# Kernel optimization log

Measured on AMD Instinct MI355X. Metric: run time of the kernel, lower is better.

## Reference

```python
import jax, jax.numpy as jnp
import numpy as np

H = 1024  # hidden_size == embedding_size


def setup_inputs() -> dict:
    key = jax.random.key(0)
    ks = jax.random.split(key, 14)
    B, T, L, V = 2, 1, 8192, 50000
    emb_table = jax.random.normal(ks[0], (V, H), jnp.float32)
    emb_table = emb_table.at[0].set(0.0)  # row 0 zeroed as in the torch module
    return {
        "input_ids": jax.random.randint(ks[1], (B, T), 0, V),
        "last_context": jax.random.normal(ks[2], (B, T, H), jnp.float32),
        "last_hidden": jax.random.normal(ks[3], (1, B, H), jnp.float32),
        "encoder_outputs": jax.random.normal(ks[4], (B, L, H), jnp.float32),
        "emb_table": emb_table,
        "w_ih": jax.random.normal(ks[5], (3 * H, 2 * H), jnp.float32) * 0.02,
        "w_hh": jax.random.normal(ks[6], (3 * H, H), jnp.float32) * 0.02,
        "b_ih": jax.random.normal(ks[7], (3 * H,), jnp.float32) * 0.02,
        "b_hh": jax.random.normal(ks[8], (3 * H,), jnp.float32) * 0.02,
        "attn_w": jax.random.normal(ks[9], (H, 2 * H), jnp.float32) * 0.02,
        "attn_b": jax.random.normal(ks[10], (H,), jnp.float32) * 0.02,
        "v": jax.random.normal(ks[11], (H,), jnp.float32),
        "out_w": jax.random.normal(ks[12], (50000, 2 * H), jnp.float32) * 0.02,
        "out_b": jax.random.normal(ks[13], (50000,), jnp.float32) * 0.02,
    }


def _forward(input_ids, last_context, last_hidden, encoder_outputs, emb_table,
             w_ih, w_hh, b_ih, b_hh, attn_w, attn_b, v, out_w, out_b):
    # Embedding lookup (dropout p=0 -> identity)
    embedded = emb_table[input_ids]                      # [B,1,H]
    rnn_in = jnp.concatenate([embedded, last_context], -1)  # [B,1,2H]

    # Single-step, single-layer GRU (torch gate order: r, z, n)
    x = rnn_in[:, 0]                                     # [B,2H]
    h = last_hidden[0]                                   # [B,H]
    gx = x @ w_ih.T + b_ih                               # [B,3H]
    gh = h @ w_hh.T + b_hh                               # [B,3H]
    r = jax.nn.sigmoid(gx[:, :H] + gh[:, :H])
    z = jax.nn.sigmoid(gx[:, H:2 * H] + gh[:, H:2 * H])
    n = jnp.tanh(gx[:, 2 * H:] + r * gh[:, 2 * H:])
    h_new = (1.0 - z) * n + z * h                        # [B,H]
    rnn_output = h_new[:, None, :]                       # [B,1,H]
    hidden = h_new[None]                                 # [1,B,H]

    # Bahdanau 'concat' attention, vectorized over the seq_len loop:
    # energy[b,i] = v . (attn_w @ concat(h_new[b], enc[b,i]) + attn_b)
    w_h, w_e = attn_w[:, :H], attn_w[:, H:]
    e_h = h_new @ w_h.T + attn_b                         # [B,H]
    e_e = jnp.einsum('blh,kh->blk', encoder_outputs, w_e)  # [B,L,H]
    energies = jnp.einsum('blk,k->bl', e_e + e_h[:, None, :], v)  # [B,L]
    attn_weights = jax.nn.softmax(energies, axis=1)      # [B,L]
    context = jnp.einsum('bl,blh->bh', attn_weights, encoder_outputs)[:, None, :]  # [B,1,H]

    # Output projection over concat(rnn_output, context)
    cat = jnp.concatenate([rnn_output, context], -1)     # [B,1,2H]
    output = cat @ out_w.T + out_b                       # [B,1,V]
    return output, context, hidden, embedded, rnn_output


def reference(input_ids, last_context, last_hidden, encoder_outputs, emb_table,
              w_ih, w_hh, b_ih, b_hh, attn_w, attn_b, v, out_w, out_b):
    return _forward(input_ids, last_context, last_hidden, encoder_outputs, emb_table,
                    w_ih, w_hh, b_ih, b_hh, attn_w, attn_b, v, out_w, out_b)
```

## Files before the change

kernel.cpp:

```cpp
#include <hip/hip_runtime.h>

#define H 1024
#define B2 2
#define LEN 8192
#define V 50000

__device__ __forceinline__ float dot4(float4 a, float4 b) {
    return a.x * b.x + a.y * b.y + a.z * b.z + a.w * b.w;
}

__global__ void k_upart_emb(const float* __restrict__ attn_w,
                            const float* __restrict__ v,
                            float* __restrict__ upart,
                            const int* __restrict__ ids,
                            const float* __restrict__ emb,
                            float* __restrict__ out_emb) {
    int bid = blockIdx.x;
    int t   = threadIdx.x;
    if (bid < 64) {
        int h  = (bid & 3) * 256 + t;
        int kc = bid >> 2;
        float acc = 0.f;
#pragma unroll 8
        for (int i = 0; i < 64; ++i) {
            int k = kc * 64 + i;
            acc += v[k] * attn_w[(long)k * (2 * H) + H + h];
        }
        upart[kc * H + h] = acc;
    } else {
        int idx = (bid - 64) * 256 + t;
        int b = idx >> 10, h = idx & 1023;
        out_emb[idx] = emb[(long)ids[b] * H + h];
    }
}

__global__ void k_ured(const float* __restrict__ upart,
                       float* __restrict__ u) {
    int h = blockIdx.x * 256 + threadIdx.x;
    float acc = 0.f;
#pragma unroll
    for (int kc = 0; kc < 16; ++kc) acc += upart[kc * H + h];
    u[h] = acc;
}

__global__ void k_gru_energy(const int* __restrict__ ids,
                             const float* __restrict__ emb,
                             const float* __restrict__ lctx,
                             const float* __restrict__ lhid,
                             const float* __restrict__ w_ih,
                             const float* __restrict__ w_hh,
                             const float* __restrict__ b_ih,
                             const float* __restrict__ b_hh,
                             const float* __restrict__ enc,
                             const float* __restrict__ u,
                             float* __restrict__ o_hidden,
                             float* __restrict__ o_rnn,
                             float* __restrict__ en) {
    __shared__ float lds[3][4][4];
    int t = threadIdx.x;

    if (blockIdx.x >= 1024) {
        int row  = ((blockIdx.x - 1024) << 2) + (t >> 6);
        int lane = t & 63;
        const float* e = enc + (long)row * H;
        float acc = 0.f;
#pragma unroll
        for (int c = 0; c < 4; ++c) {
            int k = c * 256 + lane * 4;
            float4 ev = *(const float4*)(e + k);
            float4 uv = *(const float4*)(u + k);
            acc += dot4(ev, uv);
        }
        for (int off = 32; off; off >>= 1) acc += __shfl_down(acc, off, 64);
        if (lane == 0) en[row] = acc;
        return;
    }

    int hh = blockIdx.x;
    int kb = t * 8;

    float4 x0a, x0b, x1a, x1b;
    if (kb < H) {
        const float* p0 = emb + (long)ids[0] * H + kb;
        const float* p1 = emb + (long)ids[1] * H + kb;
        x0a = *(const float4*)p0;       x0b = *(const float4*)(p0 + 4);
        x1a = *(const float4*)p1;       x1b = *(const float4*)(p1 + 4);
    } else {
        const float* p0 = lctx + (kb - H);
        const float* p1 = lctx + H + (kb - H);
        x0a = *(const float4*)p0;       x0b = *(const float4*)(p0 + 4);
        x1a = *(const float4*)p1;       x1b = *(const float4*)(p1 + 4);
    }
    int kb2 = t * 4;
    float4 h0 = *(const float4*)(lhid + kb2);
    float4 h1 = *(const float4*)(lhid + H + kb2);

    for (int g = 0; g < 3; ++g) {
        const float* wi = w_ih + ((long)g * H + hh) * (2 * H) + kb;
        const float* wh = w_hh + ((long)g * H + hh) * H + kb2;
        float4 wa = *(const float4*)wi;
        float4 wb = *(const float4*)(wi + 4);
        float4 wc = *(const float4*)wh;
        float a0 = dot4(wa, x0a) + dot4(wb, x0b);
        float a1 = dot4(wa, x1a) + dot4(wb, x1b);
        float c0 = dot4(wc, h0);
        float c1 = dot4(wc, h1);
        for (int off = 32; off; off >>= 1) {
            a0 += __shfl_down(a0, off, 64);
            a1 += __shfl_down(a1, off, 64);
            c0 += __shfl_down(c0, off, 64);
            c1 += __shfl_down(c1, off, 64);
        }
        if ((t & 63) == 0) {
            int w = t >> 6;
            lds[g][w][0] = a0; lds[g][w][1] = a1;
            lds[g][w][2] = c0; lds[g][w][3] = c1;
        }
    }
    __syncthreads();
    if (t == 0) {
        float gx[3][2], gh[3][2];
        for (int g = 0; g < 3; ++g) {
            float s0 = 0, s1 = 0, s2 = 0, s3 = 0;
            for (int w = 0; w < 4; ++w) {
                s0 += lds[g][w][0]; s1 += lds[g][w][1];
                s2 += lds[g][w][2]; s3 += lds[g][w][3];
            }
            float bi = b_ih[g * H + hh], bh = b_hh[g * H + hh];
            gx[g][0] = s0 + bi; gx[g][1] = s1 + bi;
            gh[g][0] = s2 + bh; gh[g][1] = s3 + bh;
        }
        for (int b = 0; b < B2; ++b) {
            float r  = 1.f / (1.f + expf(-(gx[0][b] + gh[0][b])));
            float z  = 1.f / (1.f + expf(-(gx[1][b] + gh[1][b])));
            float n  = tanhf(gx[2][b] + r * gh[2][b]);
            float hp = lhid[b * H + hh];
            float hn = (1.f - z) * n + z * hp;
            o_hidden[b * H + hh] = hn;
            o_rnn[b * H + hh]    = hn;
        }
    }
}

__global__ void k_ctx(const float* __restrict__ enc,
                      const float* __restrict__ en,
                      float* __restrict__ part) {
    int b  = blockIdx.x >> 7;
    int lc = blockIdx.x & 127;
    int t  = threadIdx.x;
    const float* e_row = en + b * LEN;

    __shared__ float red[4];
    __shared__ float wlds[64];

    float m = -3.4e38f;
    for (int i = t; i < LEN; i += 256) m = fmaxf(m, e_row[i]);
    for (int off = 32; off; off >>= 1) m = fmaxf(m, __shfl_xor(m, off, 64));
    if ((t & 63) == 0) red[t >> 6] = m;
    __syncthreads();
    m = fmaxf(fmaxf(red[0], red[1]), fmaxf(red[2], red[3]));

    float s = 0.f;
    for (int i = t; i < LEN; i += 256) s += expf(e_row[i] - m);
    for (int off = 32; off; off >>= 1) s += __shfl_xor(s, off, 64);
    __syncthreads();
    if ((t & 63) == 0) red[t >> 6] = s;
    __syncthreads();
    float inv = 1.f / (red[0] + red[1] + red[2] + red[3]);

    if (t < 64) wlds[t] = expf(e_row[lc * 64 + t] - m) * inv;
    __syncthreads();

    const float* e = enc + ((long)b * LEN + lc * 64) * H + t * 4;
    float4 acc = {0.f, 0.f, 0.f, 0.f};
#pragma unroll 4
    for (int i = 0; i < 64; ++i) {
        float w = wlds[i];
        float4 ev = *(const float4*)(e + (long)i * H);
        acc.x += w * ev.x; acc.y += w * ev.y; acc.z += w * ev.z; acc.w += w * ev.w;
    }
    *(float4*)(part + (long)blockIdx.x * H + t * 4) = acc;
}

__global__ void k_ctx_red(const float* __restrict__ part,
                          float* __restrict__ out_ctx) {
    int idx = blockIdx.x * 256 + threadIdx.x;
    int b = idx >> 10, h = idx & 1023;
    float acc = 0.f;
#pragma unroll 8
    for (int lc = 0; lc < 128; ++lc) acc += part[((b << 7) + lc) * H + h];
    out_ctx[idx] = acc;
}

__global__ void k_out(const float* __restrict__ ow,
                      const float* __restrict__ ob,
                      const float* __restrict__ hnew,
                      const float* __restrict__ ctx,
                      float* __restrict__ out) {
    int t    = threadIdx.x;
    int lane = t & 63;
    int wv   = t >> 6;
    long row = (long)blockIdx.x * 4 + wv;

    float4 c0[8], c1[8];
#pragma unroll
    for (int j = 0; j < 4; ++j) {
        int k = (lane + 64 * j) * 4;
        c0[j] = *(const float4*)(hnew + k);
        c1[j] = *(const float4*)(hnew + H + k);
    }
#pragma unroll
    for (int j = 4; j < 8; ++j) {
        int k = (lane + 64 * j) * 4 - H;
        c0[j] = *(const float4*)(ctx + k);
        c1[j] = *(const float4*)(ctx + H + k);
    }

    const float4* w4 = (const float4*)(ow + row * (2 * H));
    float a0 = 0.f, a1 = 0.f;
#pragma unroll
    for (int j = 0; j < 8; ++j) {
        float4 w = w4[lane + 64 * j];
        a0 += dot4(w, c0[j]);
        a1 += dot4(w, c1[j]);
    }
    for (int off = 32; off; off >>= 1) {
        a0 += __shfl_down(a0, off, 64);
        a1 += __shfl_down(a1, off, 64);
    }
    if (lane == 0) {
        float bb = ob[row];
        out[row]     = a0 + bb;
        out[V + row] = a1 + bb;
    }
}

extern "C" void kernel_launch(void* const* d_in, const int* in_sizes, int n_in,
                              void* d_out, int out_size, void* d_ws, size_t ws_size,
                              hipStream_t stream) {
    const int*   ids    = (const int*)  d_in[0];
    const float* lctx   = (const float*)d_in[1];
    const float* lhid   = (const float*)d_in[2];
    const float* enc    = (const float*)d_in[3];
    const float* emb    = (const float*)d_in[4];
    const float* w_ih   = (const float*)d_in[5];
    const float* w_hh   = (const float*)d_in[6];
    const float* b_ih   = (const float*)d_in[7];
    const float* b_hh   = (const float*)d_in[8];
    const float* attn_w = (const float*)d_in[9];
    const float* v      = (const float*)d_in[11];
    const float* out_w  = (const float*)d_in[12];
    const float* out_b  = (const float*)d_in[13];

    float* out_f       = (float*)d_out;
    float* o_output    = out_f;
    float* o_context   = out_f + 100000;
    float* o_hidden    = out_f + 102048;
    float* o_embedded  = out_f + 104096;
    float* o_rnn       = out_f + 106144;

    float* ws    = (float*)d_ws;
    float* U     = ws;
    float* UPART = ws + 1024;
    float* EN    = ws + 17408;
    float* PART  = ws + 33792;

    k_upart_emb <<<72,    256, 0, stream>>>(attn_w, v, UPART, ids, emb, o_embedded);
    k_ured      <<<4,     256, 0, stream>>>(UPART, U);
    k_gru_energy<<<5120,  256, 0, stream>>>(ids, emb, lctx, lhid, w_ih, w_hh,
                                            b_ih, b_hh, enc, U,
                                            o_hidden, o_rnn, EN);
    k_ctx       <<<256,   256, 0, stream>>>(enc, EN, PART);
    k_ctx_red   <<<8,     256, 0, stream>>>(PART, o_context);
    k_out       <<<12500, 256, 0, stream>>>(out_w, out_b, o_hidden, o_context,
                                            o_output);
}
```

Baseline: 131.6 us.

## Regroup kernel stages, fold u reduction in-block, split ctx finer, stage cat in LDS

The u = v·W_e reduction now finishes inside one block through LDS, which removes the k_ured launch. The GRU step moves into the same pre-kernel so it no longer shares a launch with the energy computation, and energy becomes its own kernel. The context pass splits into twice as many blocks with 32 rows each, for more parallelism, at the cost of a longer partial-sum reduction. The output projection stages the concatenated vectors in shared memory and has each wave process four rows, which cuts redundant global loads of hnew and ctx per block.

```diff
diff --git a/kernel.cpp b/kernel.cpp
--- a/kernel.cpp
+++ b/kernel.cpp
@@ -9,74 +9,53 @@
     return a.x * b.x + a.y * b.y + a.z * b.z + a.w * b.w;
 }
 
-__global__ void k_upart_emb(const float* __restrict__ attn_w,
-                            const float* __restrict__ v,
-                            float* __restrict__ upart,
-                            const int* __restrict__ ids,
-                            const float* __restrict__ emb,
-                            float* __restrict__ out_emb) {
+__global__ void k_pre(const float* __restrict__ attn_w,
+                      const float* __restrict__ v,
+                      float* __restrict__ u,
+                      const int* __restrict__ ids,
+                      const float* __restrict__ emb,
+                      float* __restrict__ out_emb,
+                      const float* __restrict__ lctx,
+                      const float* __restrict__ lhid,
+                      const float* __restrict__ w_ih,
+                      const float* __restrict__ w_hh,
+                      const float* __restrict__ b_ih,
+                      const float* __restrict__ b_hh,
+                      float* __restrict__ o_hidden,
+                      float* __restrict__ o_rnn) {
+    __shared__ float red[16][16];
+    __shared__ float lds[3][4][4];
     int bid = blockIdx.x;
     int t   = threadIdx.x;
+
     if (bid < 64) {
-        int h  = (bid & 3) * 256 + t;
-        int kc = bid >> 2;
+        int kg = t >> 4;
+        int hi = t & 15;
+        int h  = bid * 16 + hi;
         float acc = 0.f;
 #pragma unroll 8
         for (int i = 0; i < 64; ++i) {
-            int k = kc * 64 + i;
+            int k = kg * 64 + i;
             acc += v[k] * attn_w[(long)k * (2 * H) + H + h];
         }
-        upart[kc * H + h] = acc;
-    } else {
+        red[kg][hi] = acc;
+        __syncthreads();
+        if (t < 16) {
+            float s = 0.f;
+#pragma unroll
+            for (int g = 0; g < 16; ++g) s += red[g][t];
+            u[bid * 16 + t] = s;
+        }
+        return;
+    }
+    if (bid < 72) {
         int idx = (bid - 64) * 256 + t;
         int b = idx >> 10, h = idx & 1023;
         out_emb[idx] = emb[(long)ids[b] * H + h];
-    }
-}
-
-__global__ void k_ured(const float* __restrict__ upart,
-                       float* __restrict__ u) {
-    int h = blockIdx.x * 256 + threadIdx.x;
-    float acc = 0.f;
-#pragma unroll
-    for (int kc = 0; kc < 16; ++kc) acc += upart[kc * H + h];
-    u[h] = acc;
-}
-
-__global__ void k_gru_energy(const int* __restrict__ ids,
-                             const float* __restrict__ emb,
-                             const float* __restrict__ lctx,
-                             const float* __restrict__ lhid,
-                             const float* __restrict__ w_ih,
-                             const float* __restrict__ w_hh,
-                             const float* __restrict__ b_ih,
-                             const float* __restrict__ b_hh,
-                             const float* __restrict__ enc,
-                             const float* __restrict__ u,
-                             float* __restrict__ o_hidden,
-                             float* __restrict__ o_rnn,
-                             float* __restrict__ en) {
-    __shared__ float lds[3][4][4];
-    int t = threadIdx.x;
-
-    if (blockIdx.x >= 1024) {
-        int row  = ((blockIdx.x - 1024) << 2) + (t >> 6);
-        int lane = t & 63;
-        const float* e = enc + (long)row * H;
-        float acc = 0.f;
-#pragma unroll
-        for (int c = 0; c < 4; ++c) {
-            int k = c * 256 + lane * 4;
-            float4 ev = *(const float4*)(e + k);
-            float4 uv = *(const float4*)(u + k);
-            acc += dot4(ev, uv);
-        }
-        for (int off = 32; off; off >>= 1) acc += __shfl_down(acc, off, 64);
-        if (lane == 0) en[row] = acc;
         return;
     }
 
-    int hh = blockIdx.x;
+    int hh = bid - 72;
     int kb = t * 8;
 
     float4 x0a, x0b, x1a, x1b;
@@ -142,18 +121,37 @@
     }
 }
 
+__global__ void k_energy(const float* __restrict__ enc,
+                         const float* __restrict__ u,
+                         float* __restrict__ en) {
+    int row  = (blockIdx.x << 2) + (threadIdx.x >> 6);
+    int lane = threadIdx.x & 63;
+    const float* e = enc + (long)row * H;
+    float acc = 0.f;
+#pragma unroll
+    for (int c = 0; c < 4; ++c) {
+        int k = c * 256 + lane * 4;
+        float4 ev = *(const float4*)(e + k);
+        float4 uv = *(const float4*)(u + k);
+        acc += dot4(ev, uv);
+    }
+    for (int off = 32; off; off >>= 1) acc += __shfl_down(acc, off, 64);
+    if (lane == 0) en[row] = acc;
+}
+
 __global__ void k_ctx(const float* __restrict__ enc,
                       const float* __restrict__ en,
                       float* __restrict__ part) {
-    int b  = blockIdx.x >> 7;
-    int lc = blockIdx.x & 127;
+    int b  = blockIdx.x >> 8;
+    int lc = blockIdx.x & 255;
     int t  = threadIdx.x;
     const float* e_row = en + b * LEN;
 
     __shared__ float red[4];
-    __shared__ float wlds[64];
+    __shared__ float wlds[32];
 
     float m = -3.4e38f;
+#pragma unroll 8
     for (int i = t; i < LEN; i += 256) m = fmaxf(m, e_row[i]);
     for (int off = 32; off; off >>= 1) m = fmaxf(m, __shfl_xor(m, off, 64));
     if ((t & 63) == 0) red[t >> 6] = m;
@@ -161,6 +159,7 @@
     m = fmaxf(fmaxf(red[0], red[1]), fmaxf(red[2], red[3]));
 
     float s = 0.f;
+#pragma unroll 8
     for (int i = t; i < LEN; i += 256) s += expf(e_row[i] - m);
     for (int off = 32; off; off >>= 1) s += __shfl_xor(s, off, 64);
     __syncthreads();
@@ -168,13 +167,13 @@
     __syncthreads();
     float inv = 1.f / (red[0] + red[1] + red[2] + red[3]);
 
-    if (t < 64) wlds[t] = expf(e_row[lc * 64 + t] - m) * inv;
-    __syncthreads();
-
-    const float* e = enc + ((long)b * LEN + lc * 64) * H + t * 4;
+    if (t < 32) wlds[t] = expf(e_row[lc * 32 + t] - m) * inv;
+    __syncthreads();
+
+    const float* e = enc + ((long)b * LEN + lc * 32) * H + t * 4;
     float4 acc = {0.f, 0.f, 0.f, 0.f};
-#pragma unroll 4
-    for (int i = 0; i < 64; ++i) {
+#pragma unroll 8
+    for (int i = 0; i < 32; ++i) {
         float w = wlds[i];
         float4 ev = *(const float4*)(e + (long)i * H);
         acc.x += w * ev.x; acc.y += w * ev.y; acc.z += w * ev.z; acc.w += w * ev.w;
@@ -188,50 +187,64 @@
     int b = idx >> 10, h = idx & 1023;
     float acc = 0.f;
 #pragma unroll 8
-    for (int lc = 0; lc < 128; ++lc) acc += part[((b << 7) + lc) * H + h];
+    for (int lc = 0; lc < 256; ++lc) acc += part[(long)((b << 8) + lc) * H + h];
     out_ctx[idx] = acc;
 }
 
-__global__ void k_out(const float* __restrict__ ow,
-                      const float* __restrict__ ob,
-                      const float* __restrict__ hnew,
-                      const float* __restrict__ ctx,
-                      float* __restrict__ out) {
-    int t    = threadIdx.x;
+__global__ void __launch_bounds__(256)
+k_out(const float* __restrict__ ow,
+      const float* __restrict__ ob,
+      const float* __restrict__ hnew,
+      const float* __restrict__ ctx,
+      float* __restrict__ out) {
+    __shared__ float cat0[2 * H];
+    __shared__ float cat1[2 * H];
+    int t = threadIdx.x;
+    {
+        float4* c0 = (float4*)cat0;
+        float4* c1 = (float4*)cat1;
+#pragma unroll
+        for (int r = 0; r < 2; ++r) {
+            int idx = t + r * 256;
+            int k   = idx * 4;
+            if (k < H) {
+                c0[idx] = *(const float4*)(hnew + k);
+                c1[idx] = *(const float4*)(hnew + H + k);
+            } else {
+                c0[idx] = *(const float4*)(ctx + (k - H));
+                c1[idx] = *(const float4*)(ctx + H + (k - H));
+            }
+        }
+    }
+    __syncthreads();
+
     int lane = t & 63;
     int wv   = t >> 6;
-    long row = (long)blockIdx.x * 4 + wv;
-
-    float4 c0[8], c1[8];
-#pragma unroll
-    for (int j = 0; j < 4; ++j) {
-        int k = (lane + 64 * j) * 4;
-        c0[j] = *(const float4*)(hnew + k);
-        c1[j] = *(const float4*)(hnew + H + k);
-    }
-#pragma unroll
-    for (int j = 4; j < 8; ++j) {
-        int k = (lane + 64 * j) * 4 - H;
-        c0[j] = *(const float4*)(ctx + k);
-        c1[j] = *(const float4*)(ctx + H + k);
-    }
-
-    const float4* w4 = (const float4*)(ow + row * (2 * H));
-    float a0 = 0.f, a1 = 0.f;
-#pragma unroll
-    for (int j = 0; j < 8; ++j) {
-        float4 w = w4[lane + 64 * j];
-        a0 += dot4(w, c0[j]);
-        a1 += dot4(w, c1[j]);
-    }
-    for (int off = 32; off; off >>= 1) {
-        a0 += __shfl_down(a0, off, 64);
-        a1 += __shfl_down(a1, off, 64);
-    }
-    if (lane == 0) {
-        float bb = ob[row];
-        out[row]     = a0 + bb;
-        out[V + row] = a1 + bb;
+    long rbase = (long)blockIdx.x * 16 + wv * 4;
+    const float4* l0 = (const float4*)cat0;
+    const float4* l1 = (const float4*)cat1;
+
+    for (int r = 0; r < 4; ++r) {
+        long row = rbase + r;
+        const float4* w4 = (const float4*)(ow + row * (2 * H));
+        float a0 = 0.f, a1 = 0.f;
+#pragma unroll
+        for (int j = 0; j < 8; ++j) {
+            float4 w  = w4[lane + 64 * j];
+            float4 v0 = l0[lane + 64 * j];
+            float4 v1 = l1[lane + 64 * j];
+            a0 += dot4(w, v0);
+            a1 += dot4(w, v1);
+        }
+        for (int off = 32; off; off >>= 1) {
+            a0 += __shfl_down(a0, off, 64);
+            a1 += __shfl_down(a1, off, 64);
+        }
+        if (lane == 0) {
+            float bb = ob[row];
+            out[row]     = a0 + bb;
+            out[V + row] = a1 + bb;
+        }
     }
 }
 
@@ -259,19 +272,17 @@
     float* o_embedded  = out_f + 104096;
     float* o_rnn       = out_f + 106144;
 
-    float* ws    = (float*)d_ws;
-    float* U     = ws;
-    float* UPART = ws + 1024;
-    float* EN    = ws + 17408;
-    float* PART  = ws + 33792;
-
-    k_upart_emb <<<72,    256, 0, stream>>>(attn_w, v, UPART, ids, emb, o_embedded);
-    k_ured      <<<4,     256, 0, stream>>>(UPART, U);
-    k_gru_energy<<<5120,  256, 0, stream>>>(ids, emb, lctx, lhid, w_ih, w_hh,
-                                            b_ih, b_hh, enc, U,
-                                            o_hidden, o_rnn, EN);
-    k_ctx       <<<256,   256, 0, stream>>>(enc, EN, PART);
-    k_ctx_red   <<<8,     256, 0, stream>>>(PART, o_context);
-    k_out       <<<12500, 256, 0, stream>>>(out_w, out_b, o_hidden, o_context,
-                                            o_output);
-}
+    float* ws   = (float*)d_ws;
+    float* U    = ws;
+    float* EN   = ws + 1024;
+    float* PART = ws + 17408;
+
+    k_pre    <<<1096, 256, 0, stream>>>(attn_w, v, U, ids, emb, o_embedded,
+                                        lctx, lhid, w_ih, w_hh, b_ih, b_hh,
+                                        o_hidden, o_rnn);
+    k_energy <<<4096, 256, 0, stream>>>(enc, U, EN);
+    k_ctx    <<<512,  256, 0, stream>>>(enc, EN, PART);
+    k_ctx_red<<<8,    256, 0, stream>>>(PART, o_context);
+    k_out    <<<3125, 256, 0, stream>>>(out_w, out_b, o_hidden, o_context,
+                                        o_output);
+}
```

Measured after the change: 136.6 us. 1.04x slower.
